# Kernel optimization log

Measured on AMD Instinct MI355X. Metric: run time of the kernel, lower is better.

The kernel has to match this reference:

```python
import jax, jax.numpy as jnp
import numpy as np

E, B, D, N = 8, 4096, 128, 8192  # experts, batch, feature dim, num_stars


def setup_inputs() -> dict:
    key = jax.random.key(0)
    k1, k2 = jax.random.split(key, 2)
    x = jax.random.normal(k1, (B, D), dtype=jnp.float32)
    # E independent Dense(num_stars) heads: glorot-ish scale
    W = jax.random.normal(k2, (E, D, N), dtype=jnp.float32) * (1.0 / np.sqrt(D))
    b = jnp.zeros((E, N), dtype=jnp.float32)
    # thetaDict: E disjoint contiguous intervals over the range of x[:,0]
    edges = np.linspace(-5.0, 5.0, E + 1).astype(np.float32)
    theta_low = jnp.asarray(edges[:-1])
    theta_high = jnp.asarray(edges[1:])
    return {"x": x, "W": W, "b": b, "theta_low": theta_low, "theta_high": theta_high}


def reference(x, W, b, theta_low, theta_high):
    # th1 = x[:, 0]; cond_i = (th1 > low_i) & (th1 <= high_i)
    th1 = x[:, 0]                                              # [B]
    cond = (th1[None, :] > theta_low[:, None]) & (th1[None, :] <= theta_high[:, None])  # [E, B]
    # compute ALL expert branches densely (faithful to original wasteful compute)
    logits = jnp.einsum('bd,edn->ebn', x, W) + b[:, None, :]   # [E, B, N]
    probs = jax.nn.softmax(logits, axis=-1)                    # [E, B, N]
    idx = jnp.argmax(cond, axis=0)                             # [B] first-true index
    valid = jnp.any(cond, axis=0)                              # [B]
    sel = probs[idx, jnp.arange(x.shape[0])]                   # [B, N]
    return jnp.where(valid[:, None], sel, jnp.zeros((), dtype=sel.dtype))
```

## Files before the change

### kernel.cpp

```cpp
#include <hip/hip_runtime.h>
#include <hip/hip_fp16.h>
#include <math.h>


#define B_ROWS 4096
#define D_DIM  128
#define N_DIM  8192
#define E_NUM  8

typedef __attribute__((ext_vector_type(8))) __bf16 bf16x8;
typedef __attribute__((ext_vector_type(4))) float  f32x4;

__device__ __forceinline__ unsigned short f2bf(float f) {
    unsigned int u = __float_as_uint(f);
    unsigned int r = u + 0x7FFFu + ((u >> 16) & 1u);
    return (unsigned short)(r >> 16);
}


__global__ __launch_bounds__(1024)
void bin_kernel(const float* __restrict__ x,
                const float* __restrict__ tlo,
                const float* __restrict__ thi,
                int* __restrict__ ws_i, int m_tile) {
    __shared__ int cnt_s[E_NUM];
    __shared__ int off_s[E_NUM];
    __shared__ int cur_s[E_NUM];
    __shared__ int e_row[B_ROWS];

    int tid = threadIdx.x;
    if (tid < E_NUM) cnt_s[tid] = 0;
    __syncthreads();

    for (int r = tid; r < B_ROWS; r += 1024) {
        float th = x[(size_t)r * D_DIM];
        int e = -1;
        #pragma unroll
        for (int i = 0; i < E_NUM; ++i) {
            if (e < 0 && th > tlo[i] && th <= thi[i]) e = i;
        }
        e_row[r] = e;
        if (e >= 0) atomicAdd(&cnt_s[e], 1);
    }
    __syncthreads();

    if (tid == 0) {
        int off = 0;
        for (int e = 0; e < E_NUM; ++e) {
            ws_i[448 + e] = cnt_s[e];
            off_s[e] = off;
            cur_s[e] = off;
            off += cnt_s[e];
        }
        int nt = 0;
        for (int e = 0; e < E_NUM; ++e) {
            int c = cnt_s[e];
            int s = off_s[e];
            for (int t0 = 0; t0 < c && nt < 72; t0 += m_tile) {
                ws_i[8 + nt]   = e;
                ws_i[96 + nt]  = s + t0;
                ws_i[184 + nt] = (c - t0 < m_tile) ? (c - t0) : m_tile;
                ++nt;
            }
        }
        ws_i[0] = nt;
    }
    __syncthreads();

    for (int r = tid; r < B_ROWS; r += 1024) {
        int e = e_row[r];
        if (e >= 0) {
            int p = atomicAdd(&cur_s[e], 1);
            ws_i[512 + p] = r;
        }
    }
}

__global__ __launch_bounds__(256)
void convert_kernel(const float* __restrict__ W,
                    const int* __restrict__ ws_i,
                    unsigned short* __restrict__ wh) {
    int bid = blockIdx.x;
    int t = threadIdx.x;
    int e = bid >> 7;
    if (ws_i[448 + e] == 0) return;
    int n0 = (bid & 127) * 64;
    __shared__ __align__(16) unsigned short hi_s[64 * 136];
    const float* Wp = W + (size_t)e * D_DIM * N_DIM + n0;
    #pragma unroll
    for (int i = 0; i < 8; ++i) {
        int idx = i * 256 + t;
        int d  = idx >> 4;
        int j4 = idx & 15;
        float4 v = *(const float4*)(Wp + (size_t)d * N_DIM + j4 * 4);
        float fv[4] = {v.x, v.y, v.z, v.w};
        #pragma unroll
        for (int c = 0; c < 4; ++c) {
            int row = j4 * 4 + c;
            int dsw = d ^ (((row >> 2) & 7) << 3);
            hi_s[row * 136 + dsw] = f2bf(fv[c]);
        }
    }
    __syncthreads();
    unsigned short* whp = wh + ((size_t)e * N_DIM + n0) * D_DIM;
    #pragma unroll
    for (int i = 0; i < 4; ++i) {
        int idx = i * 256 + t;
        int nl = idx >> 4;
        int ck = idx & 15;
        int cks = ck ^ ((nl >> 2) & 7);
        *(uint4*)(whp + (size_t)nl * D_DIM + ck * 8) = *(const uint4*)(&hi_s[nl * 136 + cks * 8]);
    }
}

__global__ __launch_bounds__(512)
void gemm_mfma(const float* __restrict__ x,
               const unsigned short* __restrict__ wh,
               const float* __restrict__ bias, const int* __restrict__ ws_i,
               float* __restrict__ out) {
    int bt = blockIdx.y;
    if (bt >= ws_i[0]) return;
    int e   = ws_i[8 + bt];
    int seg = ws_i[96 + bt];
    int cnt = ws_i[184 + bt];
    const int* sorted = ws_i + 512;

    __shared__ __align__(16) unsigned short a_s[128 * 128];

    int tid = threadIdx.x;
    #pragma unroll
    for (int i = 0; i < 4; ++i) {
        int idx = i * 512 + tid;
        int row = idx >> 4;
        int ck  = idx & 15;
        unsigned short hq[8] = {0, 0, 0, 0, 0, 0, 0, 0};
        if (row < cnt) {
            int r = sorted[seg + row];
            const float* xp = x + (size_t)r * D_DIM + ck * 8;
            float4 va = *(const float4*)(xp);
            float4 vb = *(const float4*)(xp + 4);
            hq[0] = f2bf(va.x); hq[1] = f2bf(va.y); hq[2] = f2bf(va.z); hq[3] = f2bf(va.w);
            hq[4] = f2bf(vb.x); hq[5] = f2bf(vb.y); hq[6] = f2bf(vb.z); hq[7] = f2bf(vb.w);
        }
        int boff = row * 256 + ((ck * 16) ^ ((row & 7) << 4));
        *(uint4*)((char*)a_s + boff) = *(const uint4*)hq;
    }
    __syncthreads();

    int lane = tid & 63;
    int wave = tid >> 6;
    int wm = wave >> 2, wn = wave & 3;
    int l15 = lane & 15, q = lane >> 4;
    int colbase = blockIdx.x * 128 + wn * 32;

    const unsigned short* whp = wh + (size_t)e * N_DIM * D_DIM;

    f32x4 acc[4][2];
    #pragma unroll
    for (int mi = 0; mi < 4; ++mi) {
        acc[mi][0] = (f32x4){0.f, 0.f, 0.f, 0.f};
        acc[mi][1] = (f32x4){0.f, 0.f, 0.f, 0.f};
    }

    const unsigned short* base0 = whp + (size_t)(colbase + l15) * D_DIM + q * 8;

    bf16x8 b0[4], b1[4];
    #pragma unroll
    for (int s = 0; s < 4; ++s) {
        b0[s] = *(const bf16x8*)(base0 + s * 32);
        b1[s] = *(const bf16x8*)(base0 + s * 32 + 16 * D_DIM);
    }

    #pragma unroll
    for (int s = 0; s < 4; ++s) {
        const int kb = (s * 32 + q * 8) * 2;
        #pragma unroll
        for (int mi = 0; mi < 4; ++mi) {
            int row  = wm * 64 + mi * 16 + l15;
            int aoff = row * 256 + (kb ^ ((row & 7) << 4));
            bf16x8 a = *(const bf16x8*)((const char*)a_s + aoff);
            acc[mi][0] = __builtin_amdgcn_mfma_f32_16x16x32_bf16(a, b0[s], acc[mi][0], 0, 0, 0);
            acc[mi][1] = __builtin_amdgcn_mfma_f32_16x16x32_bf16(a, b1[s], acc[mi][1], 0, 0, 0);
        }
    }

    const float* bp = bias + (size_t)e * N_DIM;
    float bv0 = bp[colbase + l15];
    float bv1 = bp[colbase + 16 + l15];

    #pragma unroll
    for (int mi = 0; mi < 4; ++mi) {
        #pragma unroll
        for (int reg = 0; reg < 4; ++reg) {
            int m = wm * 64 + mi * 16 + q * 4 + reg;
            if (m < cnt) {
                int r = sorted[seg + m];
                __half* lp = (__half*)(out + (size_t)r * N_DIM);
                lp[colbase + l15]      = __float2half(acc[mi][0][reg] + bv0);
                lp[colbase + 16 + l15] = __float2half(acc[mi][1][reg] + bv1);
            }
        }
    }
}

__global__ __launch_bounds__(256)
void softmax_f16(const float* __restrict__ x,
                 const float* __restrict__ tlo,
                 const float* __restrict__ thi,
                 float* __restrict__ out) {
    int r = blockIdx.x;
    int tid = threadIdx.x;
    float th = x[(size_t)r * D_DIM];
    bool valid = false;
    #pragma unroll
    for (int i = 0; i < E_NUM; ++i) {
        if (th > tlo[i] && th <= thi[i]) valid = true;
    }
    float* row = out + (size_t)r * N_DIM;

    if (!valid) {
        float4 z = make_float4(0.f, 0.f, 0.f, 0.f);
        #pragma unroll
        for (int c = 0; c < 4; ++c) {
            *(float4*)(row + c * 2048 + tid * 8)     = z;
            *(float4*)(row + c * 2048 + tid * 8 + 4) = z;
        }
        return;
    }

    float vv[32];
    float mx = -INFINITY;
    const __half* hp = (const __half*)row;
    #pragma unroll
    for (int c = 0; c < 4; ++c) {
        uint4 u = *(const uint4*)(hp + c * 2048 + tid * 8);
        const __half2* h2 = (const __half2*)&u;
        #pragma unroll
        for (int j = 0; j < 4; ++j) {
            float2 f = __half22float2(h2[j]);
            vv[c * 8 + 2 * j]     = f.x;
            vv[c * 8 + 2 * j + 1] = f.y;
            mx = fmaxf(mx, fmaxf(f.x, f.y));
        }
    }

    __shared__ float red[8];
    #pragma unroll
    for (int o = 1; o < 64; o <<= 1) mx = fmaxf(mx, __shfl_xor(mx, o));
    if ((tid & 63) == 0) red[tid >> 6] = mx;
    __syncthreads();
    mx = fmaxf(fmaxf(red[0], red[1]), fmaxf(red[2], red[3]));

    float sum = 0.f;
    #pragma unroll
    for (int i = 0; i < 32; ++i) {
        vv[i] = expf(vv[i] - mx);
        sum += vv[i];
    }
    #pragma unroll
    for (int o = 1; o < 64; o <<= 1) sum += __shfl_xor(sum, o);
    if ((tid & 63) == 0) red[4 + (tid >> 6)] = sum;
    __syncthreads();
    sum = red[4] + red[5] + red[6] + red[7];

    float inv = 1.0f / sum;
    #pragma unroll
    for (int c = 0; c < 4; ++c) {
        float4 o0, o1;
        o0.x = vv[c * 8 + 0] * inv; o0.y = vv[c * 8 + 1] * inv;
        o0.z = vv[c * 8 + 2] * inv; o0.w = vv[c * 8 + 3] * inv;
        o1.x = vv[c * 8 + 4] * inv; o1.y = vv[c * 8 + 5] * inv;
        o1.z = vv[c * 8 + 6] * inv; o1.w = vv[c * 8 + 7] * inv;
        *(float4*)(row + c * 2048 + tid * 8)     = o0;
        *(float4*)(row + c * 2048 + tid * 8 + 4) = o1;
    }
}


__device__ __forceinline__ void fma4(float4& ac, float xs, const float4& wv) {
    ac.x = fmaf(xs, wv.x, ac.x);
    ac.y = fmaf(xs, wv.y, ac.y);
    ac.z = fmaf(xs, wv.z, ac.z);
    ac.w = fmaf(xs, wv.w, ac.w);
}

__global__ __launch_bounds__(256)
void gemm_kernel(const float* __restrict__ x,
                 const float* __restrict__ W,
                 const float* __restrict__ bias,
                 const int* __restrict__ ws_i,
                 float* __restrict__ out) {
    int bt = blockIdx.y;
    if (bt >= ws_i[0]) return;
    int e   = ws_i[8 + bt];
    int seg = ws_i[96 + bt];
    int cnt = ws_i[184 + bt];
    const int* sorted = ws_i + 512;

    __shared__ float x_s[64][D_DIM];
    __shared__ int   rows_s[64];

    int tid = threadIdx.x;
    if (tid < 64) rows_s[tid] = (tid < cnt) ? sorted[seg + tid] : -1;
    __syncthreads();

    #pragma unroll
    for (int c = 0; c < 8; ++c) {
        int idx = c * 256 + tid;
        int i = idx >> 5;
        int k4 = idx & 31;
        int r = rows_s[i];
        float4 v;
        if (r >= 0) v = *(const float4*)(x + (size_t)r * D_DIM + k4 * 4);
        else        v = make_float4(0.f, 0.f, 0.f, 0.f);
        *(float4*)(&x_s[i][k4 * 4]) = v;
    }
    __syncthreads();

    int nidx = tid & 63;
    int mg   = tid >> 6;
    int col  = blockIdx.x * 256 + nidx * 4;
    const float* Wp = W + ((size_t)e * D_DIM) * N_DIM + col;

    float4 acc[16];
    #pragma unroll
    for (int i = 0; i < 16; ++i) acc[i] = make_float4(0.f, 0.f, 0.f, 0.f);

    for (int k = 0; k < D_DIM; k += 4) {
        float4 w0 = *(const float4*)(Wp + (size_t)(k + 0) * N_DIM);
        float4 w1 = *(const float4*)(Wp + (size_t)(k + 1) * N_DIM);
        float4 w2 = *(const float4*)(Wp + (size_t)(k + 2) * N_DIM);
        float4 w3 = *(const float4*)(Wp + (size_t)(k + 3) * N_DIM);
        #pragma unroll
        for (int i = 0; i < 16; ++i) {
            float4 xv = *(const float4*)(&x_s[mg * 16 + i][k]);
            fma4(acc[i], xv.x, w0);
            fma4(acc[i], xv.y, w1);
            fma4(acc[i], xv.z, w2);
            fma4(acc[i], xv.w, w3);
        }
    }

    float4 bv = *(const float4*)(bias + (size_t)e * N_DIM + col);
    #pragma unroll
    for (int i = 0; i < 16; ++i) {
        int m = mg * 16 + i;
        if (m < cnt) {
            int r = rows_s[m];
            float4 o = acc[i];
            o.x += bv.x; o.y += bv.y; o.z += bv.z; o.w += bv.w;
            *(float4*)(out + (size_t)r * N_DIM + col) = o;
        }
    }
}

__global__ __launch_bounds__(256)
void softmax_kernel(const float* __restrict__ x,
                    const float* __restrict__ tlo,
                    const float* __restrict__ thi,
                    float* __restrict__ out) {
    int r = blockIdx.x;
    int tid = threadIdx.x;
    float th = x[(size_t)r * D_DIM];
    bool valid = false;
    #pragma unroll
    for (int i = 0; i < E_NUM; ++i) {
        if (th > tlo[i] && th <= thi[i]) valid = true;
    }
    float* row = out + (size_t)r * N_DIM;

    if (!valid) {
        float4 z = make_float4(0.f, 0.f, 0.f, 0.f);
        #pragma unroll
        for (int c = 0; c < 8; ++c)
            *(float4*)(row + c * 1024 + tid * 4) = z;
        return;
    }

    float4 v[8];
    float mx = -INFINITY;
    #pragma unroll
    for (int c = 0; c < 8; ++c) {
        v[c] = *(const float4*)(row + c * 1024 + tid * 4);
        mx = fmaxf(mx, fmaxf(fmaxf(v[c].x, v[c].y), fmaxf(v[c].z, v[c].w)));
    }

    __shared__ float red[8];
    #pragma unroll
    for (int o = 1; o < 64; o <<= 1) mx = fmaxf(mx, __shfl_xor(mx, o));
    if ((tid & 63) == 0) red[tid >> 6] = mx;
    __syncthreads();
    mx = fmaxf(fmaxf(red[0], red[1]), fmaxf(red[2], red[3]));

    float sum = 0.f;
    #pragma unroll
    for (int c = 0; c < 8; ++c) {
        v[c].x = expf(v[c].x - mx);
        v[c].y = expf(v[c].y - mx);
        v[c].z = expf(v[c].z - mx);
        v[c].w = expf(v[c].w - mx);
        sum += v[c].x + v[c].y + v[c].z + v[c].w;
    }
    #pragma unroll
    for (int o = 1; o < 64; o <<= 1) sum += __shfl_xor(sum, o);
    if ((tid & 63) == 0) red[4 + (tid >> 6)] = sum;
    __syncthreads();
    sum = red[4] + red[5] + red[6] + red[7];

    float inv = 1.0f / sum;
    #pragma unroll
    for (int c = 0; c < 8; ++c) {
        float4 o;
        o.x = v[c].x * inv; o.y = v[c].y * inv;
        o.z = v[c].z * inv; o.w = v[c].w * inv;
        *(float4*)(row + c * 1024 + tid * 4) = o;
    }
}

extern "C" void kernel_launch(void* const* d_in, const int* in_sizes, int n_in,
                              void* d_out, int out_size, void* d_ws, size_t ws_size,
                              hipStream_t stream) {
    const float* x   = (const float*)d_in[0];
    const float* W   = (const float*)d_in[1];
    const float* b   = (const float*)d_in[2];
    const float* tlo = (const float*)d_in[3];
    const float* thi = (const float*)d_in[4];
    float* out = (float*)d_out;
    int* ws_i = (int*)d_ws;

    const size_t meta = 65536;
    const size_t wsz = (size_t)E_NUM * N_DIM * D_DIM;
    unsigned short* wh = (unsigned short*)((char*)d_ws + meta);
    size_t need = meta + wsz * sizeof(unsigned short);
    bool fast = (ws_size >= need);

    bin_kernel<<<1, 1024, 0, stream>>>(x, tlo, thi, ws_i, fast ? 128 : 64);
    if (fast) {
        convert_kernel<<<1024, 256, 0, stream>>>(W, ws_i, wh);
        gemm_mfma<<<dim3(N_DIM / 128, 40), 512, 0, stream>>>(x, wh, b, ws_i, out);
        softmax_f16<<<B_ROWS, 256, 0, stream>>>(x, tlo, thi, out);
    } else {
        gemm_kernel<<<dim3(N_DIM / 256, 72), 256, 0, stream>>>(x, W, b, ws_i, out);
        softmax_kernel<<<B_ROWS, 256, 0, stream>>>(x, tlo, thi, out);
    }
}
```

Baseline: 98.27 us.

## Fuse binning into weight-convert launch and stage GEMM output through LDS for coalesced stores

Binning now runs as an extra block inside the weight-conversion kernel, which removes a separate single-block launch and its serialization ahead of conversion. The conversion no longer skips experts with zero rows, because the counts are not ready when the convert blocks run. The GEMM epilogue writes fp16 logits into swizzled shared memory and then issues 16-byte row-contiguous global stores instead of scattered 2-byte stores. The cost is an extra barrier and an LDS round trip in the epilogue.

```diff
diff --git a/kernel.cpp b/kernel.cpp
--- a/kernel.cpp
+++ b/kernel.cpp
@@ -18,98 +18,94 @@
 }
 
 
-__global__ __launch_bounds__(1024)
-void bin_kernel(const float* __restrict__ x,
-                const float* __restrict__ tlo,
-                const float* __restrict__ thi,
-                int* __restrict__ ws_i, int m_tile) {
-    __shared__ int cnt_s[E_NUM];
-    __shared__ int off_s[E_NUM];
-    __shared__ int cur_s[E_NUM];
-    __shared__ int e_row[B_ROWS];
-
-    int tid = threadIdx.x;
-    if (tid < E_NUM) cnt_s[tid] = 0;
-    __syncthreads();
-
-    for (int r = tid; r < B_ROWS; r += 1024) {
-        float th = x[(size_t)r * D_DIM];
-        int e = -1;
-        #pragma unroll
-        for (int i = 0; i < E_NUM; ++i) {
-            if (e < 0 && th > tlo[i] && th <= thi[i]) e = i;
-        }
-        e_row[r] = e;
-        if (e >= 0) atomicAdd(&cnt_s[e], 1);
-    }
-    __syncthreads();
-
-    if (tid == 0) {
-        int off = 0;
-        for (int e = 0; e < E_NUM; ++e) {
-            ws_i[448 + e] = cnt_s[e];
-            off_s[e] = off;
-            cur_s[e] = off;
-            off += cnt_s[e];
-        }
-        int nt = 0;
-        for (int e = 0; e < E_NUM; ++e) {
-            int c = cnt_s[e];
-            int s = off_s[e];
-            for (int t0 = 0; t0 < c && nt < 72; t0 += m_tile) {
-                ws_i[8 + nt]   = e;
-                ws_i[96 + nt]  = s + t0;
-                ws_i[184 + nt] = (c - t0 < m_tile) ? (c - t0) : m_tile;
-                ++nt;
-            }
-        }
-        ws_i[0] = nt;
-    }
-    __syncthreads();
-
-    for (int r = tid; r < B_ROWS; r += 1024) {
-        int e = e_row[r];
-        if (e >= 0) {
-            int p = atomicAdd(&cur_s[e], 1);
-            ws_i[512 + p] = r;
-        }
-    }
-}
-
 __global__ __launch_bounds__(256)
-void convert_kernel(const float* __restrict__ W,
-                    const int* __restrict__ ws_i,
-                    unsigned short* __restrict__ wh) {
+void convert_bin_kernel(const float* __restrict__ x, const float* __restrict__ W,
+                        const float* __restrict__ tlo, const float* __restrict__ thi,
+                        int* __restrict__ ws_i, unsigned short* __restrict__ wh) {
+    __shared__ __align__(16) unsigned short shbuf[64 * 136];
     int bid = blockIdx.x;
     int t = threadIdx.x;
-    int e = bid >> 7;
-    if (ws_i[448 + e] == 0) return;
-    int n0 = (bid & 127) * 64;
-    __shared__ __align__(16) unsigned short hi_s[64 * 136];
-    const float* Wp = W + (size_t)e * D_DIM * N_DIM + n0;
-    #pragma unroll
-    for (int i = 0; i < 8; ++i) {
-        int idx = i * 256 + t;
-        int d  = idx >> 4;
-        int j4 = idx & 15;
-        float4 v = *(const float4*)(Wp + (size_t)d * N_DIM + j4 * 4);
-        float fv[4] = {v.x, v.y, v.z, v.w};
-        #pragma unroll
-        for (int c = 0; c < 4; ++c) {
-            int row = j4 * 4 + c;
-            int dsw = d ^ (((row >> 2) & 7) << 3);
-            hi_s[row * 136 + dsw] = f2bf(fv[c]);
-        }
-    }
-    __syncthreads();
-    unsigned short* whp = wh + ((size_t)e * N_DIM + n0) * D_DIM;
-    #pragma unroll
-    for (int i = 0; i < 4; ++i) {
-        int idx = i * 256 + t;
-        int nl = idx >> 4;
-        int ck = idx & 15;
-        int cks = ck ^ ((nl >> 2) & 7);
-        *(uint4*)(whp + (size_t)nl * D_DIM + ck * 8) = *(const uint4*)(&hi_s[nl * 136 + cks * 8]);
+
+    if (bid < 1024) {
+        unsigned short* hi_s = shbuf;
+        int e = bid >> 7;
+        int n0 = (bid & 127) * 64;
+        const float* Wp = W + (size_t)e * D_DIM * N_DIM + n0;
+        #pragma unroll
+        for (int i = 0; i < 8; ++i) {
+            int idx = i * 256 + t;
+            int d  = idx >> 4;
+            int j4 = idx & 15;
+            float4 v = *(const float4*)(Wp + (size_t)d * N_DIM + j4 * 4);
+            float fv[4] = {v.x, v.y, v.z, v.w};
+            #pragma unroll
+            for (int c = 0; c < 4; ++c) {
+                int row = j4 * 4 + c;
+                int dsw = d ^ (((row >> 2) & 7) << 3);
+                hi_s[row * 136 + dsw] = f2bf(fv[c]);
+            }
+        }
+        __syncthreads();
+        unsigned short* whp = wh + ((size_t)e * N_DIM + n0) * D_DIM;
+        #pragma unroll
+        for (int i = 0; i < 4; ++i) {
+            int idx = i * 256 + t;
+            int nl = idx >> 4;
+            int ck = idx & 15;
+            int cks = ck ^ ((nl >> 2) & 7);
+            *(uint4*)(whp + (size_t)nl * D_DIM + ck * 8) = *(const uint4*)(&hi_s[nl * 136 + cks * 8]);
+        }
+    } else {
+        int* e_row = (int*)shbuf;
+        int* cnt_s = e_row + B_ROWS;
+        int* off_s = cnt_s + E_NUM;
+        int* cur_s = off_s + E_NUM;
+
+        if (t < E_NUM) cnt_s[t] = 0;
+        __syncthreads();
+
+        for (int r = t; r < B_ROWS; r += 256) {
+            float th = x[(size_t)r * D_DIM];
+            int e = -1;
+            #pragma unroll
+            for (int i = 0; i < E_NUM; ++i) {
+                if (e < 0 && th > tlo[i] && th <= thi[i]) e = i;
+            }
+            e_row[r] = e;
+            if (e >= 0) atomicAdd(&cnt_s[e], 1);
+        }
+        __syncthreads();
+
+        if (t == 0) {
+            int off = 0;
+            for (int e = 0; e < E_NUM; ++e) {
+                ws_i[448 + e] = cnt_s[e];
+                off_s[e] = off;
+                cur_s[e] = off;
+                off += cnt_s[e];
+            }
+            int nt = 0;
+            for (int e = 0; e < E_NUM; ++e) {
+                int c = cnt_s[e];
+                int s = off_s[e];
+                for (int t0 = 0; t0 < c && nt < 72; t0 += 128) {
+                    ws_i[8 + nt]   = e;
+                    ws_i[96 + nt]  = s + t0;
+                    ws_i[184 + nt] = (c - t0 < 128) ? (c - t0) : 128;
+                    ++nt;
+                }
+            }
+            ws_i[0] = nt;
+        }
+        __syncthreads();
+
+        for (int r = t; r < B_ROWS; r += 256) {
+            int e = e_row[r];
+            if (e >= 0) {
+                int p = atomicAdd(&cur_s[e], 1);
+                ws_i[512 + p] = r;
+            }
+        }
     }
 }
 
@@ -151,7 +147,7 @@
     int wave = tid >> 6;
     int wm = wave >> 2, wn = wave & 3;
     int l15 = lane & 15, q = lane >> 4;
-    int colbase = blockIdx.x * 128 + wn * 32;
+    int colbase0 = wn * 32;
 
     const unsigned short* whp = wh + (size_t)e * N_DIM * D_DIM;
 
@@ -162,7 +158,7 @@
         acc[mi][1] = (f32x4){0.f, 0.f, 0.f, 0.f};
     }
 
-    const unsigned short* base0 = whp + (size_t)(colbase + l15) * D_DIM + q * 8;
+    const unsigned short* base0 = whp + (size_t)(blockIdx.x * 128 + colbase0 + l15) * D_DIM + q * 8;
 
     bf16x8 b0[4], b1[4];
     #pragma unroll
@@ -185,20 +181,33 @@
     }
 
     const float* bp = bias + (size_t)e * N_DIM;
-    float bv0 = bp[colbase + l15];
-    float bv1 = bp[colbase + 16 + l15];
-
+    float bv0 = bp[blockIdx.x * 128 + colbase0 + l15];
+    float bv1 = bp[blockIdx.x * 128 + colbase0 + 16 + l15];
+
+    __syncthreads();
+    __half* hs = (__half*)a_s;
     #pragma unroll
     for (int mi = 0; mi < 4; ++mi) {
         #pragma unroll
         for (int reg = 0; reg < 4; ++reg) {
             int m = wm * 64 + mi * 16 + q * 4 + reg;
-            if (m < cnt) {
-                int r = sorted[seg + m];
-                __half* lp = (__half*)(out + (size_t)r * N_DIM);
-                lp[colbase + l15]      = __float2half(acc[mi][0][reg] + bv0);
-                lp[colbase + 16 + l15] = __float2half(acc[mi][1][reg] + bv1);
-            }
+            int sw = (m & 7) << 4;
+            hs[m * 128 + ((colbase0 + l15) ^ sw)]      = __float2half(acc[mi][0][reg] + bv0);
+            hs[m * 128 + ((colbase0 + 16 + l15) ^ sw)] = __float2half(acc[mi][1][reg] + bv1);
+        }
+    }
+    __syncthreads();
+
+    #pragma unroll
+    for (int i = 0; i < 4; ++i) {
+        int idx = i * 512 + tid;
+        int row = idx >> 4;
+        int ck  = idx & 15;
+        if (row < cnt) {
+            int r = sorted[seg + row];
+            __half* lp = (__half*)(out + (size_t)r * N_DIM);
+            int src = row * 128 + ((ck * 8) ^ ((row & 7) << 4));
+            *(uint4*)(lp + blockIdx.x * 128 + ck * 8) = *(const uint4*)(hs + src);
         }
     }
 }
@@ -276,6 +285,64 @@
     }
 }
 
+
+__global__ __launch_bounds__(1024)
+void bin_kernel(const float* __restrict__ x,
+                const float* __restrict__ tlo,
+                const float* __restrict__ thi,
+                int* __restrict__ ws_i, int m_tile) {
+    __shared__ int cnt_s[E_NUM];
+    __shared__ int off_s[E_NUM];
+    __shared__ int cur_s[E_NUM];
+    __shared__ int e_row[B_ROWS];
+
+    int tid = threadIdx.x;
+    if (tid < E_NUM) cnt_s[tid] = 0;
+    __syncthreads();
+
+    for (int r = tid; r < B_ROWS; r += 1024) {
+        float th = x[(size_t)r * D_DIM];
+        int e = -1;
+        #pragma unroll
+        for (int i = 0; i < E_NUM; ++i) {
+            if (e < 0 && th > tlo[i] && th <= thi[i]) e = i;
+        }
+        e_row[r] = e;
+        if (e >= 0) atomicAdd(&cnt_s[e], 1);
+    }
+    __syncthreads();
+
+    if (tid == 0) {
+        int off = 0;
+        for (int e = 0; e < E_NUM; ++e) {
+            ws_i[448 + e] = cnt_s[e];
+            off_s[e] = off;
+            cur_s[e] = off;
+            off += cnt_s[e];
+        }
+        int nt = 0;
+        for (int e = 0; e < E_NUM; ++e) {
+            int c = cnt_s[e];
+            int s = off_s[e];
+            for (int t0 = 0; t0 < c && nt < 72; t0 += m_tile) {
+                ws_i[8 + nt]   = e;
+                ws_i[96 + nt]  = s + t0;
+                ws_i[184 + nt] = (c - t0 < m_tile) ? (c - t0) : m_tile;
+                ++nt;
+            }
+        }
+        ws_i[0] = nt;
+    }
+    __syncthreads();
+
+    for (int r = tid; r < B_ROWS; r += 1024) {
+        int e = e_row[r];
+        if (e >= 0) {
+            int p = atomicAdd(&cur_s[e], 1);
+            ws_i[512 + p] = r;
+        }
+    }
+}
 
 __device__ __forceinline__ void fma4(float4& ac, float xs, const float4& wv) {
     ac.x = fmaf(xs, wv.x, ac.x);
@@ -434,12 +501,12 @@
     size_t need = meta + wsz * sizeof(unsigned short);
     bool fast = (ws_size >= need);
 
-    bin_kernel<<<1, 1024, 0, stream>>>(x, tlo, thi, ws_i, fast ? 128 : 64);
     if (fast) {
-        convert_kernel<<<1024, 256, 0, stream>>>(W, ws_i, wh);
+        convert_bin_kernel<<<1025, 256, 0, stream>>>(x, W, tlo, thi, ws_i, wh);
         gemm_mfma<<<dim3(N_DIM / 128, 40), 512, 0, stream>>>(x, wh, b, ws_i, out);
         softmax_f16<<<B_ROWS, 256, 0, stream>>>(x, tlo, thi, out);
     } else {
+        bin_kernel<<<1, 1024, 0, stream>>>(x, tlo, thi, ws_i, 64);
         gemm_kernel<<<dim3(N_DIM / 256, 72), 256, 0, stream>>>(x, W, b, ws_i, out);
         softmax_kernel<<<B_ROWS, 256, 0, stream>>>(x, tlo, thi, out);
     }
```

New measurement: 106.4 us. 1.08x slower.

## Fuse fp32-to-bf16 weight conversion into the MFMA GEMM kernel

Applied to the files above, without the earlier changes.

Removes the separate convert kernel and its bf16 weight copy in workspace. Each GEMM block now loads its 128x128 fp32 weight tile, converts it to bf16 into swizzled LDS and pulls B fragments into registers. It then reuses the same LDS buffer for the gathered activation tile. This saves a kernel launch and the write-then-read of the intermediate bf16 weights. In exchange, every row tile of an expert re-reads and re-converts the fp32 weights, which doubles the bytes per read and adds conversion work inside the GEMM.

```diff
diff --git a/kernel.cpp b/kernel.cpp
--- a/kernel.cpp
+++ b/kernel.cpp
@@ -76,46 +76,9 @@
     }
 }
 
-__global__ __launch_bounds__(256)
-void convert_kernel(const float* __restrict__ W,
-                    const int* __restrict__ ws_i,
-                    unsigned short* __restrict__ wh) {
-    int bid = blockIdx.x;
-    int t = threadIdx.x;
-    int e = bid >> 7;
-    if (ws_i[448 + e] == 0) return;
-    int n0 = (bid & 127) * 64;
-    __shared__ __align__(16) unsigned short hi_s[64 * 136];
-    const float* Wp = W + (size_t)e * D_DIM * N_DIM + n0;
-    #pragma unroll
-    for (int i = 0; i < 8; ++i) {
-        int idx = i * 256 + t;
-        int d  = idx >> 4;
-        int j4 = idx & 15;
-        float4 v = *(const float4*)(Wp + (size_t)d * N_DIM + j4 * 4);
-        float fv[4] = {v.x, v.y, v.z, v.w};
-        #pragma unroll
-        for (int c = 0; c < 4; ++c) {
-            int row = j4 * 4 + c;
-            int dsw = d ^ (((row >> 2) & 7) << 3);
-            hi_s[row * 136 + dsw] = f2bf(fv[c]);
-        }
-    }
-    __syncthreads();
-    unsigned short* whp = wh + ((size_t)e * N_DIM + n0) * D_DIM;
-    #pragma unroll
-    for (int i = 0; i < 4; ++i) {
-        int idx = i * 256 + t;
-        int nl = idx >> 4;
-        int ck = idx & 15;
-        int cks = ck ^ ((nl >> 2) & 7);
-        *(uint4*)(whp + (size_t)nl * D_DIM + ck * 8) = *(const uint4*)(&hi_s[nl * 136 + cks * 8]);
-    }
-}
-
 __global__ __launch_bounds__(512)
-void gemm_mfma(const float* __restrict__ x,
-               const unsigned short* __restrict__ wh,
+void gemm_conv(const float* __restrict__ x,
+               const float* __restrict__ W,
                const float* __restrict__ bias, const int* __restrict__ ws_i,
                float* __restrict__ out) {
     int bt = blockIdx.y;
@@ -125,9 +88,47 @@
     int cnt = ws_i[184 + bt];
     const int* sorted = ws_i + 512;
 
-    __shared__ __align__(16) unsigned short a_s[128 * 128];
+    __shared__ __align__(16) unsigned short s_buf[128 * 136];
 
     int tid = threadIdx.x;
+    int n0 = blockIdx.x * 128;
+
+    const float* Wp = W + (size_t)e * D_DIM * N_DIM + n0;
+    #pragma unroll
+    for (int i = 0; i < 8; ++i) {
+        int idx = i * 512 + tid;
+        int d  = idx >> 5;
+        int c4 = idx & 31;
+        float4 v = *(const float4*)(Wp + (size_t)d * N_DIM + c4 * 4);
+        float fv[4] = {v.x, v.y, v.z, v.w};
+        #pragma unroll
+        for (int c = 0; c < 4; ++c) {
+            int col = c4 * 4 + c;
+            int dsw = d ^ (((col >> 2) & 7) << 3);
+            s_buf[col * 136 + dsw] = f2bf(fv[c]);
+        }
+    }
+    __syncthreads();
+
+    int lane = tid & 63;
+    int wave = tid >> 6;
+    int wm = wave >> 2, wn = wave & 3;
+    int l15 = lane & 15, q = lane >> 4;
+    int colbase0 = wn * 32;
+    int colbase  = n0 + colbase0;
+
+    bf16x8 b0[4], b1[4];
+    #pragma unroll
+    for (int s = 0; s < 4; ++s) {
+        int d0 = s * 32 + q * 8;
+        int c0 = colbase0 + l15;
+        int c1 = colbase0 + 16 + l15;
+        b0[s] = *(const bf16x8*)(&s_buf[c0 * 136 + (d0 ^ (((c0 >> 2) & 7) << 3))]);
+        b1[s] = *(const bf16x8*)(&s_buf[c1 * 136 + (d0 ^ (((c1 >> 2) & 7) << 3))]);
+    }
+    __syncthreads();
+
+    unsigned short* a_s = s_buf;
     #pragma unroll
     for (int i = 0; i < 4; ++i) {
         int idx = i * 512 + tid;
@@ -147,28 +148,11 @@
     }
     __syncthreads();
 
-    int lane = tid & 63;
-    int wave = tid >> 6;
-    int wm = wave >> 2, wn = wave & 3;
-    int l15 = lane & 15, q = lane >> 4;
-    int colbase = blockIdx.x * 128 + wn * 32;
-
-    const unsigned short* whp = wh + (size_t)e * N_DIM * D_DIM;
-
     f32x4 acc[4][2];
     #pragma unroll
     for (int mi = 0; mi < 4; ++mi) {
         acc[mi][0] = (f32x4){0.f, 0.f, 0.f, 0.f};
         acc[mi][1] = (f32x4){0.f, 0.f, 0.f, 0.f};
-    }
-
-    const unsigned short* base0 = whp + (size_t)(colbase + l15) * D_DIM + q * 8;
-
-    bf16x8 b0[4], b1[4];
-    #pragma unroll
-    for (int s = 0; s < 4; ++s) {
-        b0[s] = *(const bf16x8*)(base0 + s * 32);
-        b1[s] = *(const bf16x8*)(base0 + s * 32 + 16 * D_DIM);
     }
 
     #pragma unroll
@@ -428,18 +412,14 @@
     float* out = (float*)d_out;
     int* ws_i = (int*)d_ws;
 
-    const size_t meta = 65536;
-    const size_t wsz = (size_t)E_NUM * N_DIM * D_DIM;
-    unsigned short* wh = (unsigned short*)((char*)d_ws + meta);
-    size_t need = meta + wsz * sizeof(unsigned short);
-    bool fast = (ws_size >= need);
-
-    bin_kernel<<<1, 1024, 0, stream>>>(x, tlo, thi, ws_i, fast ? 128 : 64);
+    bool fast = (ws_size >= 65536);
+
     if (fast) {
-        convert_kernel<<<1024, 256, 0, stream>>>(W, ws_i, wh);
-        gemm_mfma<<<dim3(N_DIM / 128, 40), 512, 0, stream>>>(x, wh, b, ws_i, out);
+        bin_kernel<<<1, 1024, 0, stream>>>(x, tlo, thi, ws_i, 128);
+        gemm_conv<<<dim3(N_DIM / 128, 40), 512, 0, stream>>>(x, W, b, ws_i, out);
         softmax_f16<<<B_ROWS, 256, 0, stream>>>(x, tlo, thi, out);
     } else {
+        bin_kernel<<<1, 1024, 0, stream>>>(x, tlo, thi, ws_i, 64);
         gemm_kernel<<<dim3(N_DIM / 256, 72), 256, 0, stream>>>(x, W, b, ws_i, out);
         softmax_kernel<<<B_ROWS, 256, 0, stream>>>(x, tlo, thi, out);
     }
```

Result: faster. 85.88 us (median of 2 runs) (-12.6%).
